# Optimization experiments

Measured on AMD Instinct MI355X. Metric: run time of the kernel, lower is better.

Reference implementation:

```python
import jax, jax.numpy as jnp
import numpy as np

B, H, L, D = 2, 16, 2048, 64

def _linear_feature_map(x, W):
    # x: [B,H,L,D], W: [H,D,E] -> relu(x @ W) per head, [B,H,L,E]
    return jax.nn.relu(jnp.einsum('bhld,hde->bhle', x, W))

def setup_inputs() -> dict:
    key = jax.random.key(0)
    ks = jax.random.split(key, 5)
    return {
        'query_states': jax.random.normal(ks[0], (B, H, L, D), dtype=jnp.float32),
        'key_states':   jax.random.normal(ks[1], (B, H, L, D), dtype=jnp.float32),
        'value_states': jax.random.normal(ks[2], (B, H, L, D), dtype=jnp.float32),
        'fm_q_weight':  jax.random.normal(ks[3], (H, D, D), dtype=jnp.float32),
        'fm_k_weight':  jax.random.normal(ks[4], (H, D, D), dtype=jnp.float32),
    }

def reference(query_states, key_states, value_states, fm_q_weight, fm_k_weight):
    # NOTE: source applies feature_map_k to queries and feature_map_q to keys (swapped); keep faithful.
    fq = _linear_feature_map(query_states, fm_k_weight)  # [B,H,L,D]
    fk = _linear_feature_map(key_states, fm_q_weight)    # [B,H,L,D]
    attn = jnp.einsum('bhld,bhkd->bhlk', fq, fk)         # [B,H,L,L]
    attn = jnp.tril(attn)                                # causal mask (attention_mask=None path)
    attn = attn / jnp.sum(attn, axis=-1, keepdims=True)  # row-normalize
    out = jnp.einsum('bhlk,bhkd->bhld', attn, value_states)
    return (out, attn)
```

## Files before the change

### kernel.cpp

```cpp
#include <hip/hip_runtime.h>
#include <hip/hip_bf16.h>

#define BB 2
#define HH 16
#define LL 2048
#define DD 64
constexpr int BH = BB * HH;
constexpr int NT = LL / 64;

typedef __attribute__((ext_vector_type(8))) short bf16x8;
typedef __attribute__((ext_vector_type(4))) float f32x4;

typedef unsigned short u16;
typedef unsigned int u32;

__device__ __forceinline__ u16 f2bf(float x) {
    __bf16 b = (__bf16)x;
    u16 u; __builtin_memcpy(&u, &b, 2);
    return u;
}
__device__ __forceinline__ float bf2f(u16 u) {
    union { u32 i; float f; } c; c.i = ((u32)u) << 16; return c.f;
}

__device__ __forceinline__ void gll16(const void* gptr, void* ldsptr) {
    __builtin_amdgcn_global_load_lds(
        (const u32 __attribute__((address_space(1)))*)gptr,
        (u32 __attribute__((address_space(3)))*)ldsptr, 16, 0, 0);
}

__device__ __forceinline__ bf16x8 ld_frag(const char* tile, int row, int kbyte) {
    return *(const bf16x8*)(tile + row * 128 + (kbyte ^ ((row & 7) << 4)));
}

template<bool TSUM, bool VPREP>
__global__ __launch_bounds__(256) void fmap2_kernel(
    const float* __restrict__ x, const float* __restrict__ W,
    u16* __restrict__ ghi, float* __restrict__ tsum,
    const float* __restrict__ v, u16* __restrict__ vt)
{
    __shared__ float sXT[64][64];
    __shared__ float sW[64][64];
    int bx = blockIdx.x;
    int bh = bx / NT, rb = bx % NT;
    int h = bh % HH;
    const float* xp = x + (size_t)bh * LL * DD + (size_t)rb * 64 * DD;
    const float* wp = W + (size_t)h * DD * DD;

    int tid = threadIdx.x;
    {
        int r = tid >> 2, c0 = (tid & 3) * 16;
        for (int u = 0; u < 16; u += 4) {
            float4 t = *(const float4*)(xp + r * DD + c0 + u);
            sXT[c0 + u + 0][r] = t.x; sXT[c0 + u + 1][r] = t.y;
            sXT[c0 + u + 2][r] = t.z; sXT[c0 + u + 3][r] = t.w;
            *(float4*)(&sW[r][c0 + u]) = *(const float4*)(wp + r * DD + c0 + u);
        }
    }
    __syncthreads();

    int ty = tid >> 4, tx = tid & 15;
    float acc[4][4] = {};
    #pragma unroll 4
    for (int d = 0; d < 64; ++d) {
        float4 a = *(const float4*)(&sXT[d][ty * 4]);
        float4 b = *(const float4*)(&sW[d][tx * 4]);
        float av[4] = {a.x, a.y, a.z, a.w};
        float bv[4] = {b.x, b.y, b.z, b.w};
        #pragma unroll
        for (int j = 0; j < 4; ++j)
            #pragma unroll
            for (int i = 0; i < 4; ++i)
                acc[j][i] = fmaf(av[j], bv[i], acc[j][i]);
    }

    char* hib = (char*)ghi + (size_t)bx * 8192;
    float colsum[4] = {0.f, 0.f, 0.f, 0.f};
    #pragma unroll
    for (int j = 0; j < 4; ++j) {
        int rr = ty * 4 + j;
        ushort4 hv;
        hv.x = f2bf(fmaxf(acc[j][0], 0.f));
        hv.y = f2bf(fmaxf(acc[j][1], 0.f));
        hv.z = f2bf(fmaxf(acc[j][2], 0.f));
        hv.w = f2bf(fmaxf(acc[j][3], 0.f));
        int off = rr * 128 + ((tx * 8) ^ ((rr & 7) << 4));
        *(ushort4*)(hib + off) = hv;
        if constexpr (TSUM) {
            colsum[0] += bf2f(hv.x); colsum[1] += bf2f(hv.y);
            colsum[2] += bf2f(hv.z); colsum[3] += bf2f(hv.w);
        }
    }

    if constexpr (TSUM) {
        __syncthreads();
        #pragma unroll
        for (int i = 0; i < 4; ++i)
            sXT[ty][tx * 4 + i] = colsum[i];
        __syncthreads();
        if (tid < 64) {
            float s = 0.f;
            #pragma unroll
            for (int y = 0; y < 16; ++y) s += sXT[y][tid];
            tsum[(size_t)bx * 64 + tid] = s;
        }
    }

    if constexpr (VPREP) {
        int c0 = (tid >> 4) * 4, e0 = (tid & 15) * 4;
        const float* vp = v + ((size_t)bh * LL + (size_t)rb * 64) * DD;
        float ld[4][4];
        #pragma unroll
        for (int j = 0; j < 4; ++j) {
            float4 f = *(const float4*)(vp + (size_t)(c0 + j) * DD + e0);
            ld[j][0] = f.x; ld[j][1] = f.y; ld[j][2] = f.z; ld[j][3] = f.w;
        }
        char* base = (char*)vt + (size_t)bx * 8192;
        #pragma unroll
        for (int i = 0; i < 4; ++i) {
            int e = e0 + i;
            ushort4 wv;
            wv.x = f2bf(ld[0][i]); wv.y = f2bf(ld[1][i]);
            wv.z = f2bf(ld[2][i]); wv.w = f2bf(ld[3][i]);
            *(ushort4*)(base + e * 128 + ((c0 * 2) ^ ((e & 7) << 4))) = wv;
        }
    }
}

__global__ __launch_bounds__(256) void rowsum_kernel(
    const u16* __restrict__ khi, const u16* __restrict__ qhi,
    const float* __restrict__ tsum, float* __restrict__ rinv)
{
    __shared__ float wsum[4][64];
    int bx = blockIdx.x;
    int bh = bx >> 5, t = bx & 31;
    int w = threadIdx.x >> 6, d = threadIdx.x & 63;
    const size_t tb = ((size_t)bh * NT + t) * 4096;

    float fkv[16];
    float s = 0.f;
    #pragma unroll
    for (int i = 0; i < 16; ++i) {
        int r = w * 16 + i;
        size_t idx = tb + r * 64 + (d ^ ((r & 7) << 3));
        fkv[i] = bf2f(khi[idx]);
        s += fkv[i];
    }
    wsum[w][d] = s;
    __syncthreads();

    float cs = 0.f;
    for (int t2 = 0; t2 < t; ++t2)
        cs += tsum[((size_t)bh * NT + t2) * 64 + d];
    for (int w2 = 0; w2 < w; ++w2) cs += wsum[w2][d];

    #pragma unroll
    for (int i = 0; i < 16; ++i) {
        int r = w * 16 + i;
        size_t idx = tb + r * 64 + (d ^ ((r & 7) << 3));
        cs += fkv[i];
        float tt = bf2f(qhi[idx]) * cs;
        #pragma unroll
        for (int o = 1; o < 64; o <<= 1) tt += __shfl_xor(tt, o);
        if (d == 0) rinv[(size_t)bh * LL + t * 64 + r] = 1.0f / tt;
    }
}

__global__ __launch_bounds__(256, 4) void attn5_kernel(
    const u16* __restrict__ qhi, const u16* __restrict__ khi,
    const u16* __restrict__ vt, const float* __restrict__ rinvg,
    float* __restrict__ outO, float* __restrict__ outA)
{
    __shared__ __align__(16) char lds[40960];
    char* sS = lds + 32768;

    int bx = blockIdx.x;
    int bh = bx & 31;
    int p = bx >> 5;

    int tid = threadIdx.x;
    int w = tid >> 6, l = tid & 63;
    int l15 = l & 15, lq = l >> 4;
    int o = tid * 16, wb = w << 10;

    for (int half = 0; half < 2; ++half) {
        int rblk = half ? (31 - p) : p;
        int brow = rblk * 64;

        {
            const char* qT = (const char*)qhi + ((size_t)bh * NT + rblk) * 8192;
            gll16(qT + o,        lds + 16384 + wb);
            gll16(qT + o + 4096, lds + 16384 + wb + 4096);

            const char* kT = (const char*)khi + (size_t)bh * NT * 8192;
            const char* vT = (const char*)vt  + (size_t)bh * NT * 8192;
            gll16(kT + o,        lds + wb);
            gll16(kT + o + 4096, lds + wb + 4096);
            gll16(vT + o,        lds + 8192 + wb);
            gll16(vT + o + 4096, lds + 8192 + wb + 4096);
        }
        float ri = rinvg[(size_t)bh * LL + brow + w * 16 + l15];
        asm volatile("s_waitcnt vmcnt(0)" ::: "memory");
        __syncthreads();

        int qrow = w * 16 + l15;
        bf16x8 bq[2];
        #pragma unroll
        for (int ks = 0; ks < 2; ++ks)
            bq[ks] = ld_frag(lds + 16384, qrow, lq * 16 + ks * 64);
        __syncthreads();

        f32x4 acc2[4];
        #pragma unroll
        for (int eb = 0; eb < 4; ++eb) acc2[eb] = (f32x4){0.f, 0.f, 0.f, 0.f};

        for (int ct = 0; ct <= rblk; ++ct) {
            char* cur = lds + (ct & 1) * 16384;

            if (ct < rblk) {
                char* nxt = lds + ((ct + 1) & 1) * 16384;
                const char* kT = (const char*)khi + ((size_t)bh * NT + ct + 1) * 8192;
                const char* vT = (const char*)vt  + ((size_t)bh * NT + ct + 1) * 8192;
                gll16(kT + o,        nxt + wb);
                gll16(kT + o + 4096, nxt + wb + 4096);
                gll16(vT + o,        nxt + 8192 + wb);
                gll16(vT + o + 4096, nxt + 8192 + wb + 4096);
            }

            f32x4 sa[4];
            #pragma unroll
            for (int cb = 0; cb < 4; ++cb) sa[cb] = (f32x4){0.f, 0.f, 0.f, 0.f};
            #pragma unroll
            for (int ks = 0; ks < 2; ++ks) {
                #pragma unroll
                for (int cb = 0; cb < 4; ++cb) {
                    bf16x8 ah = ld_frag(cur, cb * 16 + l15, lq * 16 + ks * 64);
                    sa[cb] = __builtin_amdgcn_mfma_f32_16x16x32_bf16(ah, bq[ks], sa[cb], 0, 0, 0);
                }
            }

            bool diag = (ct == rblk);
            int srow = w * 16 + l15;
            #pragma unroll
            for (int cb = 0; cb < 4; ++cb) {
                if (diag) {
                    #pragma unroll
                    for (int rg = 0; rg < 4; ++rg)
                        if (cb * 16 + lq * 4 + rg > srow) sa[cb][rg] = 0.f;
                }
                sa[cb] *= ri;
                ushort4 pv;
                pv.x = f2bf(sa[cb][0]); pv.y = f2bf(sa[cb][1]);
                pv.z = f2bf(sa[cb][2]); pv.w = f2bf(sa[cb][3]);
                int soff = srow * 128 + ((cb * 32 + lq * 8) ^ ((srow & 7) << 4));
                *(ushort4*)(sS + soff) = pv;
            }

            asm volatile("s_waitcnt lgkmcnt(0)" ::: "memory");
            __builtin_amdgcn_sched_barrier(0);
            __builtin_amdgcn_s_barrier();
            __builtin_amdgcn_sched_barrier(0);

            {
                int bcol = ct * 64;
                float* atile = outA + ((size_t)bh * LL + brow) * LL + bcol;
                #pragma unroll
                for (int u = 0; u < 4; ++u) {
                    int idx = tid + u * 256;
                    int r = idx >> 4;
                    int c = idx & 15;
                    ushort4 pv = *(const ushort4*)(sS + r * 128 + ((c * 8) ^ ((r & 7) << 4)));
                    f32x4 o4 = { bf2f(pv.x), bf2f(pv.y), bf2f(pv.z), bf2f(pv.w) };
                    __builtin_nontemporal_store(o4, (f32x4*)(atile + (size_t)r * LL + c * 4));
                }
            }

            bf16x8 pf[2];
            #pragma unroll
            for (int ks = 0; ks < 2; ++ks)
                pf[ks] = ld_frag(sS, srow, lq * 16 + ks * 64);
            #pragma unroll
            for (int ks = 0; ks < 2; ++ks) {
                #pragma unroll
                for (int eb = 0; eb < 4; ++eb) {
                    bf16x8 av = ld_frag(cur + 8192, eb * 16 + l15, lq * 16 + ks * 64);
                    acc2[eb] = __builtin_amdgcn_mfma_f32_16x16x32_bf16(av, pf[ks], acc2[eb], 0, 0, 0);
                }
            }

            __syncthreads();
        }

        f32x4 z = {0.f, 0.f, 0.f, 0.f};
        for (int ct2 = rblk + 1; ct2 < NT; ++ct2) {
            int bcol = ct2 * 64;
            #pragma unroll
            for (int u = 0; u < 4; ++u) {
                int idx = tid + u * 256;
                int r = idx >> 4, c4 = idx & 15;
                __builtin_nontemporal_store(z,
                    (f32x4*)(outA + ((size_t)bh * LL + brow + r) * LL + bcol + c4 * 4));
            }
        }

        float* oo = outO + ((size_t)bh * LL + brow + w * 16 + l15) * DD;
        #pragma unroll
        for (int eb = 0; eb < 4; ++eb) {
            float4 o4 = { acc2[eb][0], acc2[eb][1], acc2[eb][2], acc2[eb][3] };
            *(float4*)(oo + eb * 16 + lq * 4) = o4;
        }
    }
}

extern "C" void kernel_launch(void* const* d_in, const int* in_sizes, int n_in,
                              void* d_out, int out_size, void* d_ws, size_t ws_size,
                              hipStream_t stream)
{
    (void)in_sizes; (void)n_in; (void)out_size; (void)ws_size;
    const float* q  = (const float*)d_in[0];
    const float* k  = (const float*)d_in[1];
    const float* v  = (const float*)d_in[2];
    const float* Wq = (const float*)d_in[3];
    const float* Wk = (const float*)d_in[4];

    float* out  = (float*)d_out;
    float* attn = out + (size_t)BB * HH * LL * DD;

    const size_t TILE_HW = (size_t)BH * NT * 4096;
    u16* QHI = (u16*)d_ws;
    u16* KHI = QHI + TILE_HW;
    u16* VT  = KHI + TILE_HW;
    float* RINV = (float*)(VT + TILE_HW);
    float* TSUM = RINV + (size_t)BH * LL;

    fmap2_kernel<false, true><<<BH * NT, 256, 0, stream>>>(q, Wk, QHI, nullptr, v, VT);
    fmap2_kernel<true, false><<<BH * NT, 256, 0, stream>>>(k, Wq, KHI, TSUM, nullptr, nullptr);
    rowsum_kernel<<<BH * NT, 256, 0, stream>>>(KHI, QHI, TSUM, RINV);
    attn5_kernel<<<BH * 16, 256, 0, stream>>>(QHI, KHI, VT, RINV, out, attn);
}
```

Before: 175.1 us.

## Interleave upper-triangle zero stores into causal loop and relax barriers

The separate zero-fill pass over the upper triangle of the attention matrix now runs inside the causal tile loop, emitting one zero tile per iteration. The aim is to spread the large store stream across compute instead of bunching it at the end of each half. The attention-tile writeback now has each wave read back only its own rows of the staging buffer, which removes one block barrier per iteration. The full __syncthreads calls are replaced by explicit s_barrier with vmcnt waits that cover only the K/V prefetch loads, not the outstanding stores. The risk is that the hand-computed vmcnt counts depend on the exact order in which loads and stores are issued.

```diff
diff --git a/kernel.cpp b/kernel.cpp
--- a/kernel.cpp
+++ b/kernel.cpp
@@ -166,7 +166,7 @@
     }
 }
 
-__global__ __launch_bounds__(256, 4) void attn5_kernel(
+__global__ __launch_bounds__(256, 4) void attn6_kernel(
     const u16* __restrict__ qhi, const u16* __restrict__ khi,
     const u16* __restrict__ vt, const float* __restrict__ rinvg,
     float* __restrict__ outO, float* __restrict__ outA)
@@ -183,6 +183,10 @@
     int l15 = l & 15, lq = l >> 4;
     int o = tid * 16, wb = w << 10;
 
+    const f32x4 zvec = {0.f, 0.f, 0.f, 0.f};
+    int z = 0;
+    const int z_half0 = 31 - p;
+
     for (int half = 0; half < 2; ++half) {
         int rblk = half ? (31 - p) : p;
         int brow = rblk * 64;
@@ -200,24 +204,32 @@
             gll16(vT + o + 4096, lds + 8192 + wb + 4096);
         }
         float ri = rinvg[(size_t)bh * LL + brow + w * 16 + l15];
+        __builtin_amdgcn_sched_barrier(0);
         asm volatile("s_waitcnt vmcnt(0)" ::: "memory");
-        __syncthreads();
+        __builtin_amdgcn_sched_barrier(0);
+        __builtin_amdgcn_s_barrier();
+        __builtin_amdgcn_sched_barrier(0);
 
         int qrow = w * 16 + l15;
         bf16x8 bq[2];
         #pragma unroll
         for (int ks = 0; ks < 2; ++ks)
             bq[ks] = ld_frag(lds + 16384, qrow, lq * 16 + ks * 64);
-        __syncthreads();
+        __builtin_amdgcn_sched_barrier(0);
+        asm volatile("s_waitcnt lgkmcnt(0)" ::: "memory");
+        __builtin_amdgcn_sched_barrier(0);
+        __builtin_amdgcn_s_barrier();
+        __builtin_amdgcn_sched_barrier(0);
 
         f32x4 acc2[4];
         #pragma unroll
-        for (int eb = 0; eb < 4; ++eb) acc2[eb] = (f32x4){0.f, 0.f, 0.f, 0.f};
+        for (int eb = 0; eb < 4; ++eb) acc2[eb] = zvec;
 
         for (int ct = 0; ct <= rblk; ++ct) {
             char* cur = lds + (ct & 1) * 16384;
-
-            if (ct < rblk) {
+            bool willload = (ct < rblk);
+
+            if (willload) {
                 char* nxt = lds + ((ct + 1) & 1) * 16384;
                 const char* kT = (const char*)khi + ((size_t)bh * NT + ct + 1) * 8192;
                 const char* vT = (const char*)vt  + ((size_t)bh * NT + ct + 1) * 8192;
@@ -226,10 +238,11 @@
                 gll16(vT + o,        nxt + 8192 + wb);
                 gll16(vT + o + 4096, nxt + 8192 + wb + 4096);
             }
+            __builtin_amdgcn_sched_barrier(0);
 
             f32x4 sa[4];
             #pragma unroll
-            for (int cb = 0; cb < 4; ++cb) sa[cb] = (f32x4){0.f, 0.f, 0.f, 0.f};
+            for (int cb = 0; cb < 4; ++cb) sa[cb] = zvec;
             #pragma unroll
             for (int ks = 0; ks < 2; ++ks) {
                 #pragma unroll
@@ -256,22 +269,15 @@
                 *(ushort4*)(sS + soff) = pv;
             }
 
-            asm volatile("s_waitcnt lgkmcnt(0)" ::: "memory");
-            __builtin_amdgcn_sched_barrier(0);
-            __builtin_amdgcn_s_barrier();
-            __builtin_amdgcn_sched_barrier(0);
-
             {
                 int bcol = ct * 64;
                 float* atile = outA + ((size_t)bh * LL + brow) * LL + bcol;
                 #pragma unroll
                 for (int u = 0; u < 4; ++u) {
-                    int idx = tid + u * 256;
-                    int r = idx >> 4;
-                    int c = idx & 15;
-                    ushort4 pv = *(const ushort4*)(sS + r * 128 + ((c * 8) ^ ((r & 7) << 4)));
+                    int r = w * 16 + u * 4 + lq;
+                    ushort4 pv = *(const ushort4*)(sS + r * 128 + ((l15 * 8) ^ ((r & 7) << 4)));
                     f32x4 o4 = { bf2f(pv.x), bf2f(pv.y), bf2f(pv.z), bf2f(pv.w) };
-                    __builtin_nontemporal_store(o4, (f32x4*)(atile + (size_t)r * LL + c * 4));
+                    __builtin_nontemporal_store(o4, (f32x4*)(atile + (size_t)r * LL + l15 * 4));
                 }
             }
 
@@ -288,19 +294,29 @@
                 }
             }
 
-            __syncthreads();
-        }
-
-        f32x4 z = {0.f, 0.f, 0.f, 0.f};
-        for (int ct2 = rblk + 1; ct2 < NT; ++ct2) {
-            int bcol = ct2 * 64;
-            #pragma unroll
-            for (int u = 0; u < 4; ++u) {
-                int idx = tid + u * 256;
-                int r = idx >> 4, c4 = idx & 15;
-                __builtin_nontemporal_store(z,
-                    (f32x4*)(outA + ((size_t)bh * LL + brow + r) * LL + bcol + c4 * 4));
-            }
+            bool had_zero = (z < 31);
+            if (had_zero) {
+                int zbrow, zcol;
+                if (z < z_half0) { zbrow = p * 64;        zcol = (p + 1 + z) * 64; }
+                else             { zbrow = (31 - p) * 64; zcol = (32 - p + (z - z_half0)) * 64; }
+                ++z;
+                #pragma unroll
+                for (int u = 0; u < 4; ++u) {
+                    int idx = tid + u * 256;
+                    int r = idx >> 4, c4 = idx & 15;
+                    __builtin_nontemporal_store(zvec,
+                        (f32x4*)(outA + ((size_t)bh * LL + zbrow + r) * LL + zcol + c4 * 4));
+                }
+            }
+
+            __builtin_amdgcn_sched_barrier(0);
+            if (willload) {
+                if (had_zero) asm volatile("s_waitcnt vmcnt(8)" ::: "memory");
+                else          asm volatile("s_waitcnt vmcnt(4)" ::: "memory");
+            }
+            __builtin_amdgcn_sched_barrier(0);
+            __builtin_amdgcn_s_barrier();
+            __builtin_amdgcn_sched_barrier(0);
         }
 
         float* oo = outO + ((size_t)bh * LL + brow + w * 16 + l15) * DD;
@@ -336,5 +352,5 @@
     fmap2_kernel<false, true><<<BH * NT, 256, 0, stream>>>(q, Wk, QHI, nullptr, v, VT);
     fmap2_kernel<true, false><<<BH * NT, 256, 0, stream>>>(k, Wq, KHI, TSUM, nullptr, nullptr);
     rowsum_kernel<<<BH * NT, 256, 0, stream>>>(KHI, QHI, TSUM, RINV);
-    attn5_kernel<<<BH * 16, 256, 0, stream>>>(QHI, KHI, VT, RINV, out, attn);
-}
+    attn6_kernel<<<BH * 16, 256, 0, stream>>>(QHI, KHI, VT, RINV, out, attn);
+}
```

After: 191.5 us. 1.09x slower.

## Use one row-block per workgroup and batch attention-tile stores through LDS

Applied to the files above, without the earlier changes.

Replaces the paired-row-block (p, 31-p) scheme with one 64-row block per workgroup, launched over BH*NT workgroups. Normalized score tiles are staged in four LDS slots and written out every four column tiles, so each wave stores 1 KB contiguous row segments (256 columns) with regular stores instead of nontemporal 256 B segments. Masked upper-triangle tiles are zeroed in LDS and written through the same path instead of a separate zero-fill loop. In exchange, LDS grows to 64 KB with launch bounds lowered to 2 per CU, workgroups get uneven amounts of work, and the write-streaming hint is dropped.

```diff
diff --git a/kernel.cpp b/kernel.cpp
--- a/kernel.cpp
+++ b/kernel.cpp
@@ -166,149 +166,140 @@
     }
 }
 
-__global__ __launch_bounds__(256, 4) void attn5_kernel(
+__global__ __launch_bounds__(256, 2) void attn7_kernel(
     const u16* __restrict__ qhi, const u16* __restrict__ khi,
     const u16* __restrict__ vt, const float* __restrict__ rinvg,
     float* __restrict__ outO, float* __restrict__ outA)
 {
-    __shared__ __align__(16) char lds[40960];
+    __shared__ __align__(16) char lds[65536];
     char* sS = lds + 32768;
 
     int bx = blockIdx.x;
     int bh = bx & 31;
-    int p = bx >> 5;
+    int rblk = bx >> 5;
+    int brow = rblk * 64;
 
     int tid = threadIdx.x;
     int w = tid >> 6, l = tid & 63;
     int l15 = l & 15, lq = l >> 4;
     int o = tid * 16, wb = w << 10;
 
-    for (int half = 0; half < 2; ++half) {
-        int rblk = half ? (31 - p) : p;
-        int brow = rblk * 64;
+    const f32x4 zvec = {0.f, 0.f, 0.f, 0.f};
+
+    {
+        const char* qT = (const char*)qhi + ((size_t)bh * NT + rblk) * 8192;
+        gll16(qT + o,        sS + wb);
+        gll16(qT + o + 4096, sS + wb + 4096);
+
+        const char* kT = (const char*)khi + (size_t)bh * NT * 8192;
+        const char* vT = (const char*)vt  + (size_t)bh * NT * 8192;
+        gll16(kT + o,        lds + wb);
+        gll16(kT + o + 4096, lds + wb + 4096);
+        gll16(vT + o,        lds + 8192 + wb);
+        gll16(vT + o + 4096, lds + 8192 + wb + 4096);
+    }
+    float ri = rinvg[(size_t)bh * LL + brow + w * 16 + l15];
+    asm volatile("s_waitcnt vmcnt(0)" ::: "memory");
+    __syncthreads();
+
+    int qrow = w * 16 + l15;
+    bf16x8 bq[2];
+    #pragma unroll
+    for (int ks = 0; ks < 2; ++ks)
+        bq[ks] = ld_frag(sS, qrow, lq * 16 + ks * 64);
+
+    f32x4 acc2[4];
+    #pragma unroll
+    for (int eb = 0; eb < 4; ++eb) acc2[eb] = zvec;
+
+    int srow = w * 16 + l15;
+
+    for (int g = 0; g < 8; ++g) {
+        #pragma unroll
+        for (int j = 0; j < 4; ++j) {
+            int ct = g * 4 + j;
+            char* slot = sS + j * 8192;
+
+            if (ct <= rblk) {
+                char* cur = lds + (ct & 1) * 16384;
+
+                if (ct < rblk) {
+                    char* nxt = lds + ((ct + 1) & 1) * 16384;
+                    const char* kT = (const char*)khi + ((size_t)bh * NT + ct + 1) * 8192;
+                    const char* vT = (const char*)vt  + ((size_t)bh * NT + ct + 1) * 8192;
+                    gll16(kT + o,        nxt + wb);
+                    gll16(kT + o + 4096, nxt + wb + 4096);
+                    gll16(vT + o,        nxt + 8192 + wb);
+                    gll16(vT + o + 4096, nxt + 8192 + wb + 4096);
+                }
+
+                f32x4 sa[4];
+                #pragma unroll
+                for (int cb = 0; cb < 4; ++cb) sa[cb] = zvec;
+                #pragma unroll
+                for (int ks = 0; ks < 2; ++ks) {
+                    #pragma unroll
+                    for (int cb = 0; cb < 4; ++cb) {
+                        bf16x8 ah = ld_frag(cur, cb * 16 + l15, lq * 16 + ks * 64);
+                        sa[cb] = __builtin_amdgcn_mfma_f32_16x16x32_bf16(ah, bq[ks], sa[cb], 0, 0, 0);
+                    }
+                }
+
+                bool diag = (ct == rblk);
+                #pragma unroll
+                for (int cb = 0; cb < 4; ++cb) {
+                    if (diag) {
+                        #pragma unroll
+                        for (int rg = 0; rg < 4; ++rg)
+                            if (cb * 16 + lq * 4 + rg > srow) sa[cb][rg] = 0.f;
+                    }
+                    sa[cb] *= ri;
+                    ushort4 pv;
+                    pv.x = f2bf(sa[cb][0]); pv.y = f2bf(sa[cb][1]);
+                    pv.z = f2bf(sa[cb][2]); pv.w = f2bf(sa[cb][3]);
+                    int soff = srow * 128 + ((cb * 32 + lq * 8) ^ ((srow & 7) << 4));
+                    *(ushort4*)(slot + soff) = pv;
+                }
+
+                bf16x8 pf[2];
+                #pragma unroll
+                for (int ks = 0; ks < 2; ++ks)
+                    pf[ks] = ld_frag(slot, srow, lq * 16 + ks * 64);
+                #pragma unroll
+                for (int ks = 0; ks < 2; ++ks) {
+                    #pragma unroll
+                    for (int eb = 0; eb < 4; ++eb) {
+                        bf16x8 av = ld_frag(cur + 8192, eb * 16 + l15, lq * 16 + ks * 64);
+                        acc2[eb] = __builtin_amdgcn_mfma_f32_16x16x32_bf16(av, pf[ks], acc2[eb], 0, 0, 0);
+                    }
+                }
+
+                asm volatile("s_waitcnt vmcnt(0)" ::: "memory");
+                __syncthreads();
+            } else {
+                *(f32x4*)(slot + w * 2048 + l * 32)      = zvec;
+                *(f32x4*)(slot + w * 2048 + l * 32 + 16) = zvec;
+            }
+        }
 
         {
-            const char* qT = (const char*)qhi + ((size_t)bh * NT + rblk) * 8192;
-            gll16(qT + o,        lds + 16384 + wb);
-            gll16(qT + o + 4096, lds + 16384 + wb + 4096);
-
-            const char* kT = (const char*)khi + (size_t)bh * NT * 8192;
-            const char* vT = (const char*)vt  + (size_t)bh * NT * 8192;
-            gll16(kT + o,        lds + wb);
-            gll16(kT + o + 4096, lds + wb + 4096);
-            gll16(vT + o,        lds + 8192 + wb);
-            gll16(vT + o + 4096, lds + 8192 + wb + 4096);
-        }
-        float ri = rinvg[(size_t)bh * LL + brow + w * 16 + l15];
-        asm volatile("s_waitcnt vmcnt(0)" ::: "memory");
-        __syncthreads();
-
-        int qrow = w * 16 + l15;
-        bf16x8 bq[2];
-        #pragma unroll
-        for (int ks = 0; ks < 2; ++ks)
-            bq[ks] = ld_frag(lds + 16384, qrow, lq * 16 + ks * 64);
-        __syncthreads();
-
-        f32x4 acc2[4];
-        #pragma unroll
-        for (int eb = 0; eb < 4; ++eb) acc2[eb] = (f32x4){0.f, 0.f, 0.f, 0.f};
-
-        for (int ct = 0; ct <= rblk; ++ct) {
-            char* cur = lds + (ct & 1) * 16384;
-
-            if (ct < rblk) {
-                char* nxt = lds + ((ct + 1) & 1) * 16384;
-                const char* kT = (const char*)khi + ((size_t)bh * NT + ct + 1) * 8192;
-                const char* vT = (const char*)vt  + ((size_t)bh * NT + ct + 1) * 8192;
-                gll16(kT + o,        nxt + wb);
-                gll16(kT + o + 4096, nxt + wb + 4096);
-                gll16(vT + o,        nxt + 8192 + wb);
-                gll16(vT + o + 4096, nxt + 8192 + wb + 4096);
+            float* abase = outA + ((size_t)bh * LL + brow) * LL + g * 256;
+            const char* src = sS + (l >> 4) * 8192;
+            #pragma unroll
+            for (int u = 0; u < 16; ++u) {
+                int r = w * 16 + u;
+                ushort4 pv = *(const ushort4*)(src + r * 128 + (((l15) * 8) ^ ((r & 7) << 4)));
+                f32x4 o4 = { bf2f(pv.x), bf2f(pv.y), bf2f(pv.z), bf2f(pv.w) };
+                *(f32x4*)(abase + (size_t)r * LL + l * 4) = o4;
             }
-
-            f32x4 sa[4];
-            #pragma unroll
-            for (int cb = 0; cb < 4; ++cb) sa[cb] = (f32x4){0.f, 0.f, 0.f, 0.f};
-            #pragma unroll
-            for (int ks = 0; ks < 2; ++ks) {
-                #pragma unroll
-                for (int cb = 0; cb < 4; ++cb) {
-                    bf16x8 ah = ld_frag(cur, cb * 16 + l15, lq * 16 + ks * 64);
-                    sa[cb] = __builtin_amdgcn_mfma_f32_16x16x32_bf16(ah, bq[ks], sa[cb], 0, 0, 0);
-                }
-            }
-
-            bool diag = (ct == rblk);
-            int srow = w * 16 + l15;
-            #pragma unroll
-            for (int cb = 0; cb < 4; ++cb) {
-                if (diag) {
-                    #pragma unroll
-                    for (int rg = 0; rg < 4; ++rg)
-                        if (cb * 16 + lq * 4 + rg > srow) sa[cb][rg] = 0.f;
-                }
-                sa[cb] *= ri;
-                ushort4 pv;
-                pv.x = f2bf(sa[cb][0]); pv.y = f2bf(sa[cb][1]);
-                pv.z = f2bf(sa[cb][2]); pv.w = f2bf(sa[cb][3]);
-                int soff = srow * 128 + ((cb * 32 + lq * 8) ^ ((srow & 7) << 4));
-                *(ushort4*)(sS + soff) = pv;
-            }
-
-            asm volatile("s_waitcnt lgkmcnt(0)" ::: "memory");
-            __builtin_amdgcn_sched_barrier(0);
-            __builtin_amdgcn_s_barrier();
-            __builtin_amdgcn_sched_barrier(0);
-
-            {
-                int bcol = ct * 64;
-                float* atile = outA + ((size_t)bh * LL + brow) * LL + bcol;
-                #pragma unroll
-                for (int u = 0; u < 4; ++u) {
-                    int idx = tid + u * 256;
-                    int r = idx >> 4;
-                    int c = idx & 15;
-                    ushort4 pv = *(const ushort4*)(sS + r * 128 + ((c * 8) ^ ((r & 7) << 4)));
-                    f32x4 o4 = { bf2f(pv.x), bf2f(pv.y), bf2f(pv.z), bf2f(pv.w) };
-                    __builtin_nontemporal_store(o4, (f32x4*)(atile + (size_t)r * LL + c * 4));
-                }
-            }
-
-            bf16x8 pf[2];
-            #pragma unroll
-            for (int ks = 0; ks < 2; ++ks)
-                pf[ks] = ld_frag(sS, srow, lq * 16 + ks * 64);
-            #pragma unroll
-            for (int ks = 0; ks < 2; ++ks) {
-                #pragma unroll
-                for (int eb = 0; eb < 4; ++eb) {
-                    bf16x8 av = ld_frag(cur + 8192, eb * 16 + l15, lq * 16 + ks * 64);
-                    acc2[eb] = __builtin_amdgcn_mfma_f32_16x16x32_bf16(av, pf[ks], acc2[eb], 0, 0, 0);
-                }
-            }
-
-            __syncthreads();
-        }
-
-        f32x4 z = {0.f, 0.f, 0.f, 0.f};
-        for (int ct2 = rblk + 1; ct2 < NT; ++ct2) {
-            int bcol = ct2 * 64;
-            #pragma unroll
-            for (int u = 0; u < 4; ++u) {
-                int idx = tid + u * 256;
-                int r = idx >> 4, c4 = idx & 15;
-                __builtin_nontemporal_store(z,
-                    (f32x4*)(outA + ((size_t)bh * LL + brow + r) * LL + bcol + c4 * 4));
-            }
-        }
-
-        float* oo = outO + ((size_t)bh * LL + brow + w * 16 + l15) * DD;
-        #pragma unroll
-        for (int eb = 0; eb < 4; ++eb) {
-            float4 o4 = { acc2[eb][0], acc2[eb][1], acc2[eb][2], acc2[eb][3] };
-            *(float4*)(oo + eb * 16 + lq * 4) = o4;
-        }
+        }
+    }
+
+    float* oo = outO + ((size_t)bh * LL + brow + w * 16 + l15) * DD;
+    #pragma unroll
+    for (int eb = 0; eb < 4; ++eb) {
+        float4 o4 = { acc2[eb][0], acc2[eb][1], acc2[eb][2], acc2[eb][3] };
+        *(float4*)(oo + eb * 16 + lq * 4) = o4;
     }
 }
 
@@ -336,5 +327,5 @@
     fmap2_kernel<false, true><<<BH * NT, 256, 0, stream>>>(q, Wk, QHI, nullptr, v, VT);
     fmap2_kernel<true, false><<<BH * NT, 256, 0, stream>>>(k, Wq, KHI, TSUM, nullptr, nullptr);
     rowsum_kernel<<<BH * NT, 256, 0, stream>>>(KHI, QHI, TSUM, RINV);
-    attn5_kernel<<<BH * 16, 256, 0, stream>>>(QHI, KHI, VT, RINV, out, attn);
-}
+    attn7_kernel<<<BH * NT, 256, 0, stream>>>(QHI, KHI, VT, RINV, out, attn);
+}
```

After: 179.9 us. 1.03x slower.

## Merge feature-map launches and fold row normalisation into attention kernel

Applied to the files above, without the earlier changes.

The two feature-map launches become one kernel that picks the Q or K branch by block index. The separate rowsum kernel is removed, and each attention block computes its own row normalisers from the diagonal K tile and the Q tile in LDS plus prefix tile sums. The attention grid changes from 16 blocks per head, each processing a paired short and long row block, to one block per row block, with a remapped block-to-head/row order for load balance and L2 locality. This cuts two launches and a global round trip for the normalisers. The costs are redundant prefix-sum reads in every block and possibly worse balance, since blocks no longer pair short and long causal work.

```diff
diff --git a/kernel.cpp b/kernel.cpp
--- a/kernel.cpp
+++ b/kernel.cpp
@@ -33,15 +33,22 @@
     return *(const bf16x8*)(tile + row * 128 + (kbyte ^ ((row & 7) << 4)));
 }
 
-template<bool TSUM, bool VPREP>
-__global__ __launch_bounds__(256) void fmap2_kernel(
-    const float* __restrict__ x, const float* __restrict__ W,
-    u16* __restrict__ ghi, float* __restrict__ tsum,
+__global__ __launch_bounds__(256) void fmap_kernel(
+    const float* __restrict__ q, const float* __restrict__ k,
+    const float* __restrict__ Wq, const float* __restrict__ Wk,
+    u16* __restrict__ QHI, u16* __restrict__ KHI,
+    float* __restrict__ tsum,
     const float* __restrict__ v, u16* __restrict__ vt)
 {
     __shared__ float sXT[64][64];
     __shared__ float sW[64][64];
-    int bx = blockIdx.x;
+    int bx0 = blockIdx.x;
+    bool isK = bx0 >= BH * NT;
+    int bx = isK ? bx0 - BH * NT : bx0;
+    const float* x = isK ? k : q;
+    const float* W = isK ? Wq : Wk;
+    u16* ghi = isK ? KHI : QHI;
+
     int bh = bx / NT, rb = bx % NT;
     int h = bh % HH;
     const float* xp = x + (size_t)bh * LL * DD + (size_t)rb * 64 * DD;
@@ -86,13 +93,13 @@
         hv.w = f2bf(fmaxf(acc[j][3], 0.f));
         int off = rr * 128 + ((tx * 8) ^ ((rr & 7) << 4));
         *(ushort4*)(hib + off) = hv;
-        if constexpr (TSUM) {
+        if (isK) {
             colsum[0] += bf2f(hv.x); colsum[1] += bf2f(hv.y);
             colsum[2] += bf2f(hv.z); colsum[3] += bf2f(hv.w);
         }
     }
 
-    if constexpr (TSUM) {
+    if (isK) {
         __syncthreads();
         #pragma unroll
         for (int i = 0; i < 4; ++i)
@@ -104,9 +111,7 @@
             for (int y = 0; y < 16; ++y) s += sXT[y][tid];
             tsum[(size_t)bx * 64 + tid] = s;
         }
-    }
-
-    if constexpr (VPREP) {
+    } else {
         int c0 = (tid >> 4) * 4, e0 = (tid & 15) * 4;
         const float* vp = v + ((size_t)bh * LL + (size_t)rb * 64) * DD;
         float ld[4][4];
@@ -127,188 +132,186 @@
     }
 }
 
-__global__ __launch_bounds__(256) void rowsum_kernel(
-    const u16* __restrict__ khi, const u16* __restrict__ qhi,
-    const float* __restrict__ tsum, float* __restrict__ rinv)
-{
-    __shared__ float wsum[4][64];
-    int bx = blockIdx.x;
-    int bh = bx >> 5, t = bx & 31;
-    int w = threadIdx.x >> 6, d = threadIdx.x & 63;
-    const size_t tb = ((size_t)bh * NT + t) * 4096;
-
-    float fkv[16];
-    float s = 0.f;
-    #pragma unroll
-    for (int i = 0; i < 16; ++i) {
-        int r = w * 16 + i;
-        size_t idx = tb + r * 64 + (d ^ ((r & 7) << 3));
-        fkv[i] = bf2f(khi[idx]);
-        s += fkv[i];
-    }
-    wsum[w][d] = s;
-    __syncthreads();
-
-    float cs = 0.f;
-    for (int t2 = 0; t2 < t; ++t2)
-        cs += tsum[((size_t)bh * NT + t2) * 64 + d];
-    for (int w2 = 0; w2 < w; ++w2) cs += wsum[w2][d];
-
-    #pragma unroll
-    for (int i = 0; i < 16; ++i) {
-        int r = w * 16 + i;
-        size_t idx = tb + r * 64 + (d ^ ((r & 7) << 3));
-        cs += fkv[i];
-        float tt = bf2f(qhi[idx]) * cs;
-        #pragma unroll
-        for (int o = 1; o < 64; o <<= 1) tt += __shfl_xor(tt, o);
-        if (d == 0) rinv[(size_t)bh * LL + t * 64 + r] = 1.0f / tt;
-    }
-}
-
-__global__ __launch_bounds__(256, 4) void attn5_kernel(
+__global__ __launch_bounds__(256, 4) void attn9_kernel(
     const u16* __restrict__ qhi, const u16* __restrict__ khi,
-    const u16* __restrict__ vt, const float* __restrict__ rinvg,
+    const u16* __restrict__ vt, const float* __restrict__ tsum,
     float* __restrict__ outO, float* __restrict__ outA)
 {
     __shared__ __align__(16) char lds[40960];
     char* sS = lds + 32768;
 
     int bx = blockIdx.x;
-    int bh = bx & 31;
-    int p = bx >> 5;
+    int bh = (bx & 7) * 4 + (bx >> 8);
+    int jj = (bx >> 3) & 31;
+    int rblk = (jj & 1) ? (jj >> 1) : (31 - (jj >> 1));
+    int brow = rblk * 64;
 
     int tid = threadIdx.x;
     int w = tid >> 6, l = tid & 63;
     int l15 = l & 15, lq = l >> 4;
     int o = tid * 16, wb = w << 10;
 
-    for (int half = 0; half < 2; ++half) {
-        int rblk = half ? (31 - p) : p;
-        int brow = rblk * 64;
+    {
+        const char* qT  = (const char*)qhi + ((size_t)bh * NT + rblk) * 8192;
+        const char* kdT = (const char*)khi + ((size_t)bh * NT + rblk) * 8192;
+        gll16(qT + o,         lds + 16384 + wb);
+        gll16(qT + o + 4096,  lds + 16384 + wb + 4096);
+        gll16(kdT + o,        lds + wb);
+        gll16(kdT + o + 4096, lds + wb + 4096);
+    }
+    asm volatile("s_waitcnt vmcnt(0)" ::: "memory");
+    __syncthreads();
+
+    int qrow = w * 16 + l15;
+    bf16x8 bq[2];
+    #pragma unroll
+    for (int ks = 0; ks < 2; ++ks)
+        bq[ks] = ld_frag(lds + 16384, qrow, lq * 16 + ks * 64);
+
+    float ri;
+    {
+        float* wsum = (float*)(lds + 8192);
+        float* sInv = (float*)(lds + 8192 + 1024);
+        float fkv[16];
+        float s = 0.f;
+        #pragma unroll
+        for (int i = 0; i < 16; ++i) {
+            int r = w * 16 + i;
+            fkv[i] = bf2f(*(const u16*)(lds + r * 128 + ((l * 2) ^ ((r & 7) << 4))));
+            s += fkv[i];
+        }
+        wsum[w * 64 + l] = s;
+        __syncthreads();
+
+        float cs = 0.f;
+        for (int t2 = 0; t2 < rblk; ++t2)
+            cs += tsum[((size_t)bh * NT + t2) * 64 + l];
+        for (int w2 = 0; w2 < w; ++w2) cs += wsum[w2 * 64 + l];
+
+        #pragma unroll
+        for (int i = 0; i < 16; ++i) {
+            int r = w * 16 + i;
+            cs += fkv[i];
+            float qv = bf2f(*(const u16*)(lds + 16384 + r * 128 + ((l * 2) ^ ((r & 7) << 4))));
+            float tt = qv * cs;
+            #pragma unroll
+            for (int o2 = 1; o2 < 64; o2 <<= 1) tt += __shfl_xor(tt, o2);
+            if (l == 0) sInv[w * 16 + i] = 1.0f / tt;
+        }
+        ri = sInv[w * 16 + l15];
+        __syncthreads();
+    }
+
+    {
+        const char* kT = (const char*)khi + (size_t)bh * NT * 8192;
+        const char* vT = (const char*)vt  + (size_t)bh * NT * 8192;
+        gll16(kT + o,        lds + wb);
+        gll16(kT + o + 4096, lds + wb + 4096);
+        gll16(vT + o,        lds + 8192 + wb);
+        gll16(vT + o + 4096, lds + 8192 + wb + 4096);
+    }
+    asm volatile("s_waitcnt vmcnt(0)" ::: "memory");
+    __syncthreads();
+
+    f32x4 acc2[4];
+    #pragma unroll
+    for (int eb = 0; eb < 4; ++eb) acc2[eb] = (f32x4){0.f, 0.f, 0.f, 0.f};
+
+    int srow = w * 16 + l15;
+
+    for (int ct = 0; ct <= rblk; ++ct) {
+        char* cur = lds + (ct & 1) * 16384;
+
+        if (ct < rblk) {
+            char* nxt = lds + ((ct + 1) & 1) * 16384;
+            const char* kT = (const char*)khi + ((size_t)bh * NT + ct + 1) * 8192;
+            const char* vT = (const char*)vt  + ((size_t)bh * NT + ct + 1) * 8192;
+            gll16(kT + o,        nxt + wb);
+            gll16(kT + o + 4096, nxt + wb + 4096);
+            gll16(vT + o,        nxt + 8192 + wb);
+            gll16(vT + o + 4096, nxt + 8192 + wb + 4096);
+        }
+
+        f32x4 sa[4];
+        #pragma unroll
+        for (int cb = 0; cb < 4; ++cb) sa[cb] = (f32x4){0.f, 0.f, 0.f, 0.f};
+        #pragma unroll
+        for (int ks = 0; ks < 2; ++ks) {
+            #pragma unroll
+            for (int cb = 0; cb < 4; ++cb) {
+                bf16x8 ah = ld_frag(cur, cb * 16 + l15, lq * 16 + ks * 64);
+                sa[cb] = __builtin_amdgcn_mfma_f32_16x16x32_bf16(ah, bq[ks], sa[cb], 0, 0, 0);
+            }
+        }
+
+        bool diag = (ct == rblk);
+        #pragma unroll
+        for (int cb = 0; cb < 4; ++cb) {
+            if (diag) {
+                #pragma unroll
+                for (int rg = 0; rg < 4; ++rg)
+                    if (cb * 16 + lq * 4 + rg > srow) sa[cb][rg] = 0.f;
+            }
+            sa[cb] *= ri;
+            ushort4 pv;
+            pv.x = f2bf(sa[cb][0]); pv.y = f2bf(sa[cb][1]);
+            pv.z = f2bf(sa[cb][2]); pv.w = f2bf(sa[cb][3]);
+            int soff = srow * 128 + ((cb * 32 + lq * 8) ^ ((srow & 7) << 4));
+            *(ushort4*)(sS + soff) = pv;
+        }
+
+        asm volatile("s_waitcnt lgkmcnt(0)" ::: "memory");
+        __builtin_amdgcn_sched_barrier(0);
+        __builtin_amdgcn_s_barrier();
+        __builtin_amdgcn_sched_barrier(0);
 
         {
-            const char* qT = (const char*)qhi + ((size_t)bh * NT + rblk) * 8192;
-            gll16(qT + o,        lds + 16384 + wb);
-            gll16(qT + o + 4096, lds + 16384 + wb + 4096);
-
-            const char* kT = (const char*)khi + (size_t)bh * NT * 8192;
-            const char* vT = (const char*)vt  + (size_t)bh * NT * 8192;
-            gll16(kT + o,        lds + wb);
-            gll16(kT + o + 4096, lds + wb + 4096);
-            gll16(vT + o,        lds + 8192 + wb);
-            gll16(vT + o + 4096, lds + 8192 + wb + 4096);
-        }
-        float ri = rinvg[(size_t)bh * LL + brow + w * 16 + l15];
-        asm volatile("s_waitcnt vmcnt(0)" ::: "memory");
-        __syncthreads();
-
-        int qrow = w * 16 + l15;
-        bf16x8 bq[2];
-        #pragma unroll
-        for (int ks = 0; ks < 2; ++ks)
-            bq[ks] = ld_frag(lds + 16384, qrow, lq * 16 + ks * 64);
-        __syncthreads();
-
-        f32x4 acc2[4];
-        #pragma unroll
-        for (int eb = 0; eb < 4; ++eb) acc2[eb] = (f32x4){0.f, 0.f, 0.f, 0.f};
-
-        for (int ct = 0; ct <= rblk; ++ct) {
-            char* cur = lds + (ct & 1) * 16384;
-
-            if (ct < rblk) {
-                char* nxt = lds + ((ct + 1) & 1) * 16384;
-                const char* kT = (const char*)khi + ((size_t)bh * NT + ct + 1) * 8192;
-                const char* vT = (const char*)vt  + ((size_t)bh * NT + ct + 1) * 8192;
-                gll16(kT + o,        nxt + wb);
-                gll16(kT + o + 4096, nxt + wb + 4096);
-                gll16(vT + o,        nxt + 8192 + wb);
-                gll16(vT + o + 4096, nxt + 8192 + wb + 4096);
-            }
-
-            f32x4 sa[4];
-            #pragma unroll
-            for (int cb = 0; cb < 4; ++cb) sa[cb] = (f32x4){0.f, 0.f, 0.f, 0.f};
-            #pragma unroll
-            for (int ks = 0; ks < 2; ++ks) {
-                #pragma unroll
-                for (int cb = 0; cb < 4; ++cb) {
-                    bf16x8 ah = ld_frag(cur, cb * 16 + l15, lq * 16 + ks * 64);
-                    sa[cb] = __builtin_amdgcn_mfma_f32_16x16x32_bf16(ah, bq[ks], sa[cb], 0, 0, 0);
-                }
-            }
-
-            bool diag = (ct == rblk);
-            int srow = w * 16 + l15;
-            #pragma unroll
-            for (int cb = 0; cb < 4; ++cb) {
-                if (diag) {
-                    #pragma unroll
-                    for (int rg = 0; rg < 4; ++rg)
-                        if (cb * 16 + lq * 4 + rg > srow) sa[cb][rg] = 0.f;
-                }
-                sa[cb] *= ri;
-                ushort4 pv;
-                pv.x = f2bf(sa[cb][0]); pv.y = f2bf(sa[cb][1]);
-                pv.z = f2bf(sa[cb][2]); pv.w = f2bf(sa[cb][3]);
-                int soff = srow * 128 + ((cb * 32 + lq * 8) ^ ((srow & 7) << 4));
-                *(ushort4*)(sS + soff) = pv;
-            }
-
-            asm volatile("s_waitcnt lgkmcnt(0)" ::: "memory");
-            __builtin_amdgcn_sched_barrier(0);
-            __builtin_amdgcn_s_barrier();
-            __builtin_amdgcn_sched_barrier(0);
-
-            {
-                int bcol = ct * 64;
-                float* atile = outA + ((size_t)bh * LL + brow) * LL + bcol;
-                #pragma unroll
-                for (int u = 0; u < 4; ++u) {
-                    int idx = tid + u * 256;
-                    int r = idx >> 4;
-                    int c = idx & 15;
-                    ushort4 pv = *(const ushort4*)(sS + r * 128 + ((c * 8) ^ ((r & 7) << 4)));
-                    f32x4 o4 = { bf2f(pv.x), bf2f(pv.y), bf2f(pv.z), bf2f(pv.w) };
-                    __builtin_nontemporal_store(o4, (f32x4*)(atile + (size_t)r * LL + c * 4));
-                }
-            }
-
-            bf16x8 pf[2];
-            #pragma unroll
-            for (int ks = 0; ks < 2; ++ks)
-                pf[ks] = ld_frag(sS, srow, lq * 16 + ks * 64);
-            #pragma unroll
-            for (int ks = 0; ks < 2; ++ks) {
-                #pragma unroll
-                for (int eb = 0; eb < 4; ++eb) {
-                    bf16x8 av = ld_frag(cur + 8192, eb * 16 + l15, lq * 16 + ks * 64);
-                    acc2[eb] = __builtin_amdgcn_mfma_f32_16x16x32_bf16(av, pf[ks], acc2[eb], 0, 0, 0);
-                }
-            }
-
-            __syncthreads();
-        }
-
-        f32x4 z = {0.f, 0.f, 0.f, 0.f};
-        for (int ct2 = rblk + 1; ct2 < NT; ++ct2) {
-            int bcol = ct2 * 64;
+            int bcol = ct * 64;
+            float* atile = outA + ((size_t)bh * LL + brow) * LL + bcol;
             #pragma unroll
             for (int u = 0; u < 4; ++u) {
                 int idx = tid + u * 256;
-                int r = idx >> 4, c4 = idx & 15;
-                __builtin_nontemporal_store(z,
-                    (f32x4*)(outA + ((size_t)bh * LL + brow + r) * LL + bcol + c4 * 4));
+                int r = idx >> 4;
+                int c = idx & 15;
+                ushort4 pv = *(const ushort4*)(sS + r * 128 + ((c * 8) ^ ((r & 7) << 4)));
+                f32x4 o4 = { bf2f(pv.x), bf2f(pv.y), bf2f(pv.z), bf2f(pv.w) };
+                __builtin_nontemporal_store(o4, (f32x4*)(atile + (size_t)r * LL + c * 4));
             }
         }
 
-        float* oo = outO + ((size_t)bh * LL + brow + w * 16 + l15) * DD;
-        #pragma unroll
-        for (int eb = 0; eb < 4; ++eb) {
-            float4 o4 = { acc2[eb][0], acc2[eb][1], acc2[eb][2], acc2[eb][3] };
-            *(float4*)(oo + eb * 16 + lq * 4) = o4;
-        }
+        bf16x8 pf[2];
+        #pragma unroll
+        for (int ks = 0; ks < 2; ++ks)
+            pf[ks] = ld_frag(sS, srow, lq * 16 + ks * 64);
+        #pragma unroll
+        for (int ks = 0; ks < 2; ++ks) {
+            #pragma unroll
+            for (int eb = 0; eb < 4; ++eb) {
+                bf16x8 av = ld_frag(cur + 8192, eb * 16 + l15, lq * 16 + ks * 64);
+                acc2[eb] = __builtin_amdgcn_mfma_f32_16x16x32_bf16(av, pf[ks], acc2[eb], 0, 0, 0);
+            }
+        }
+
+        __syncthreads();
+    }
+
+    f32x4 z = {0.f, 0.f, 0.f, 0.f};
+    for (int ct2 = rblk + 1; ct2 < NT; ++ct2) {
+        int bcol = ct2 * 64;
+        #pragma unroll
+        for (int u = 0; u < 4; ++u) {
+            int idx = tid + u * 256;
+            int r = idx >> 4, c4 = idx & 15;
+            __builtin_nontemporal_store(z,
+                (f32x4*)(outA + ((size_t)bh * LL + brow + r) * LL + bcol + c4 * 4));
+        }
+    }
+
+    float* oo = outO + ((size_t)bh * LL + brow + w * 16 + l15) * DD;
+    #pragma unroll
+    for (int eb = 0; eb < 4; ++eb) {
+        float4 o4 = { acc2[eb][0], acc2[eb][1], acc2[eb][2], acc2[eb][3] };
+        *(float4*)(oo + eb * 16 + lq * 4) = o4;
     }
 }
 
@@ -330,11 +333,8 @@
     u16* QHI = (u16*)d_ws;
     u16* KHI = QHI + TILE_HW;
     u16* VT  = KHI + TILE_HW;
-    float* RINV = (float*)(VT + TILE_HW);
-    float* TSUM = RINV + (size_t)BH * LL;
-
-    fmap2_kernel<false, true><<<BH * NT, 256, 0, stream>>>(q, Wk, QHI, nullptr, v, VT);
-    fmap2_kernel<true, false><<<BH * NT, 256, 0, stream>>>(k, Wq, KHI, TSUM, nullptr, nullptr);
-    rowsum_kernel<<<BH * NT, 256, 0, stream>>>(KHI, QHI, TSUM, RINV);
-    attn5_kernel<<<BH * 16, 256, 0, stream>>>(QHI, KHI, VT, RINV, out, attn);
-}
+    float* TSUM = (float*)(VT + TILE_HW);
+
+    fmap_kernel<<<2 * BH * NT, 256, 0, stream>>>(q, k, Wq, Wk, QHI, KHI, TSUM, v, VT);
+    attn9_kernel<<<BH * NT, 256, 0, stream>>>(QHI, KHI, VT, TSUM, out, attn);
+}
```

Result: faster. 162.7 us (-7.1%).
